# Kernel tuning notes

Measured on AMD Instinct MI355X. Metric: run time of the kernel, lower is better.

## Reference

```python
import jax, jax.numpy as jnp
import numpy as np

N_A, N_G, D, H = 100000, 25000, 128, 4
E_B, E_O, E_R, E_P = 400000, 100000, 200000, 200000
BN_INV = float(1.0 / np.sqrt(1.0 + 1e-5))  # eval-mode BatchNorm1d, running mean 0 / var 1


def setup_inputs():
    key = jax.random.key(0)
    ks = iter(jax.random.split(key, 64))
    nrm = lambda shape, s=0.05: jax.random.normal(next(ks), shape, jnp.float32) * s
    ri = lambda n, hi: jax.random.randint(next(ks), (n,), 0, hi, jnp.int32)
    inp = dict(
        x_atom=nrm((N_A, D), 1.0), x_group=nrm((N_G, D), 1.0),
        ef_bond=nrm((E_B, D), 1.0), ef_overlap=nrm((E_O, D), 1.0),
        bond_src=ri(E_B, N_A), bond_dst=ri(E_B, N_A),
        ov_src=ri(E_O, N_G), ov_dst=ri(E_O, N_G),
        ref_src=ri(E_R, N_G), ref_dst=ri(E_R, N_A),
        pool_src=ri(E_P, N_A), pool_dst=ri(E_P, N_G),
    )
    # two GINE convs (bond 'b', overlap 'o'): eps + MLP Linear(D,2D)->BN->ReLU->Linear(2D,D)
    for pre in ('b', 'o'):
        inp[pre + '_eps'] = jnp.zeros((1,), jnp.float32)
        inp[pre + '_W1'] = nrm((D, 2 * D)); inp[pre + '_b1'] = jnp.zeros((2 * D,), jnp.float32)
        inp[pre + '_g1'] = jnp.ones((2 * D,), jnp.float32); inp[pre + '_be1'] = jnp.zeros((2 * D,), jnp.float32)
        inp[pre + '_W2'] = nrm((2 * D, D)); inp[pre + '_b2'] = jnp.zeros((D,), jnp.float32)
    # two ModifiedGATConvs (refine 'r', pool 'p'): GATConv + Flatten->BN->ReLU->Linear
    for pre in ('r', 'p'):
        inp[pre + '_Wfc'] = nrm((D, H * D)); inp[pre + '_al'] = nrm((H, D)); inp[pre + '_ar'] = nrm((H, D))
        inp[pre + '_Wres'] = nrm((D, H * D)); inp[pre + '_bias'] = jnp.zeros((H * D,), jnp.float32)
        inp[pre + '_g'] = jnp.ones((H * D,), jnp.float32); inp[pre + '_b'] = jnp.zeros((H * D,), jnp.float32)
        inp[pre + '_Wout'] = nrm((H * D, D)); inp[pre + '_bout'] = jnp.zeros((D,), jnp.float32)
    return inp


def _gine(x_src, x_dst, efeat, src, dst, n_dst, eps, W1, b1, g1, be1, W2, b2):
    m = jax.nn.relu(x_src[src] + efeat)                       # [E, D] message: relu(h_src + e)
    neigh = jax.ops.segment_sum(m, dst, num_segments=n_dst)   # [Nd, D] sum-reduce
    h = (1.0 + eps) * x_dst + neigh
    h = h @ W1 + b1
    h = jax.nn.relu(g1 * (h * BN_INV) + be1)                  # eval BN
    return h @ W2 + b2


def _gat(x_src, x_dst, src, dst, n_dst, Wfc, al, ar, Wres, bias, g, b, Wout, bout):
    hs = (x_src @ Wfc).reshape(-1, H, D)                      # [Ns, H, D]
    hd = (x_dst @ Wfc).reshape(-1, H, D)
    el = jnp.sum(hs * al, axis=-1)                            # [Ns, H]
    er = jnp.sum(hd * ar, axis=-1)                            # [Nd, H]
    e = jax.nn.leaky_relu(el[src] + er[dst], 0.2)             # [E, H]
    emax = jax.ops.segment_max(e, dst, num_segments=n_dst)    # per-dst softmax (stable)
    ex = jnp.exp(e - emax[dst])
    den = jax.ops.segment_sum(ex, dst, num_segments=n_dst)
    a = ex / jnp.maximum(den[dst], 1e-9)                      # [E, H]
    rst = jax.ops.segment_sum(a[:, :, None] * hs[src], dst, num_segments=n_dst)  # [Nd, H, D]
    rst = rst + (x_dst @ Wres).reshape(-1, H, D) + bias.reshape(H, D)            # residual + bias
    flat = rst.reshape(-1, H * D)                             # Flatten
    h = jax.nn.relu(g * (flat * BN_INV) + b)                  # eval BN -> ReLU
    return h @ Wout + bout


def reference(x_atom, x_group, ef_bond, ef_overlap, bond_src, bond_dst, ov_src, ov_dst, ref_src, ref_dst, pool_src, pool_dst, b_eps, b_W1, b_b1, b_g1, b_be1, b_W2, b_b2, o_eps, o_W1, o_b1, o_g1, o_be1, o_W2, o_b2, r_Wfc, r_al, r_ar, r_Wres, r_bias, r_g, r_b, r_Wout, r_bout, p_Wfc, p_al, p_ar, p_Wres, p_bias, p_g, p_b, p_Wout, p_bout):
    # HeteroGraphConv with default 'sum' cross-relation aggregation per dst node type
    out_atom = _gine(x_atom, x_atom, ef_bond, bond_src, bond_dst, N_A, b_eps, b_W1, b_b1, b_g1, b_be1, b_W2, b_b2)
    out_atom = out_atom + _gat(x_group, x_atom, ref_src, ref_dst, N_A, r_Wfc, r_al, r_ar, r_Wres, r_bias, r_g, r_b, r_Wout, r_bout)
    out_group = _gine(x_group, x_group, ef_overlap, ov_src, ov_dst, N_G, o_eps, o_W1, o_b1, o_g1, o_be1, o_W2, o_b2)
    out_group = out_group + _gat(x_atom, x_group, pool_src, pool_dst, N_G, p_Wfc, p_al, p_ar, p_Wres, p_bias, p_g, p_b, p_Wout, p_bout)
    return jnp.concatenate([out_atom, out_group], axis=0)     # [N_A + N_G, D]
```

## Files before the change

kernel.cpp:

```cpp
#include <hip/hip_runtime.h>
#include <hip/hip_bf16.h>

#define N_A 100000
#define N_G 25000
#define DD 128
#define E_B 400000
#define E_O 100000
#define E_R 200000
#define E_P 200000
#define EALL 900000
#define NSLOT 250000
#define STRIDE 64

static constexpr float BN_INV_C = 0.99999500003749969f;

typedef __attribute__((ext_vector_type(8))) short bf16x8;
typedef __attribute__((ext_vector_type(4))) float f32x4;

__device__ __forceinline__ unsigned short f2bf(float f) {
    unsigned u = __float_as_uint(f);
    unsigned r = (u + 0x7FFFu + ((u >> 16) & 1u)) >> 16;
    return (unsigned short)r;
}
__device__ __forceinline__ float bf2f(unsigned short s) {
    return __uint_as_float(((unsigned)s) << 16);
}
__device__ __forceinline__ float lrelu(float v) { return v > 0.f ? v : 0.2f * v; }

__global__ void k_xcast_all(const float* __restrict__ xa, const float* __restrict__ xg,
                            unsigned short* __restrict__ xab, unsigned short* __restrict__ xgb) {
    int t = blockIdx.x * blockDim.x + threadIdx.x;
    if (t < N_A * 32) {
        float4 v = *(const float4*)(xa + (size_t)t * 4);
        ushort4 o; o.x = f2bf(v.x); o.y = f2bf(v.y); o.z = f2bf(v.z); o.w = f2bf(v.w);
        *(ushort4*)(xab + (size_t)t * 4) = o;
    } else {
        int t2 = t - N_A * 32;
        if (t2 >= N_G * 32) return;
        float4 v = *(const float4*)(xg + (size_t)t2 * 4);
        ushort4 o; o.x = f2bf(v.x); o.y = f2bf(v.y); o.z = f2bf(v.z); o.w = f2bf(v.w);
        *(ushort4*)(xgb + (size_t)t2 * 4) = o;
    }
}

struct WcSeg { const float* src; unsigned short* dst; int K; int N; int ldk; int off; };
struct WcArgs { WcSeg s[10]; };

__global__ void k_wcast_all(WcArgs a) {
    WcSeg sg = a.s[blockIdx.y];
    int t = blockIdx.x * blockDim.x + threadIdx.x;
    if (t >= sg.K * sg.N) return;
    int n = t % sg.N, k = t / sg.N;
    sg.dst[(size_t)n * sg.ldk + sg.off + k] = f2bf(sg.src[t]);
}

__global__ void k_war_all(const float* __restrict__ rWfc, const float* __restrict__ ral,
                          const float* __restrict__ rar, const float* __restrict__ pWfc,
                          const float* __restrict__ pal, const float* __restrict__ par,
                          float* __restrict__ wv) {
    int bsel = blockIdx.x;
    const float* W = bsel < 2 ? rWfc : pWfc;
    const float* vec = bsel == 0 ? ral : bsel == 1 ? rar : bsel == 2 ? pal : par;
    float* o = wv + bsel * 512;
    int t = threadIdx.x;
    int k = t >> 2, h = t & 3;
    const float* wr = W + (size_t)k * 512 + h * 128;
    const float* av = vec + h * 128;
    float s = 0.f;
    for (int d = 0; d < 128; ++d) s += wr[d] * av[d];
    o[t] = s;
}

__global__ void k_adj_fill(const int* __restrict__ bs, const int* __restrict__ bd,
                           const int* __restrict__ os, const int* __restrict__ od,
                           const int* __restrict__ rs, const int* __restrict__ rd,
                           const int* __restrict__ ps, const int* __restrict__ pd,
                           int* __restrict__ deg, uint2* __restrict__ adj,
                           int* __restrict__ heads, int* __restrict__ nxt) {
    int t = blockIdx.x * blockDim.x + threadIdx.x;
    int e, base, go; const int* S; const int* D;
    if (t < E_B) { e = t; S = bs; D = bd; base = 0; go = 0; }
    else if (t < E_B + E_O) { e = t - E_B; S = os; D = od; base = 100000; go = E_B; }
    else if (t < E_B + E_O + E_R) { e = t - (E_B + E_O); S = rs; D = rd; base = 125000; go = E_B + E_O; }
    else if (t < EALL) { e = t - (E_B + E_O + E_R); S = ps; D = pd; base = 225000; go = E_B + E_O + E_R; }
    else return;
    int d = D[e], s = S[e];
    int ns = base + d;
    int pos = atomicAdd(&deg[ns], 1);
    if (pos < STRIDE) adj[(size_t)ns * STRIDE + pos] = make_uint2((unsigned)e, (unsigned)s);
    else nxt[go + e] = atomicExch(&heads[ns], e);
}

__global__ __launch_bounds__(256) void k_gine_gather_all(
    const unsigned short* __restrict__ xAb, const unsigned short* __restrict__ xGb,
    const float* __restrict__ efB, const float* __restrict__ efO,
    const int* __restrict__ bsrc, const int* __restrict__ osrc,
    const int* __restrict__ deg, const uint2* __restrict__ adj,
    const int* __restrict__ heads, const int* __restrict__ nxt,
    const float* __restrict__ beps, const float* __restrict__ oeps,
    unsigned short* __restrict__ h0A, unsigned short* __restrict__ h0G) {
    int wid = threadIdx.x >> 6, lane = threadIdx.x & 63;
    int n = blockIdx.x * 4 + wid;
    __shared__ uint2 gl[4][STRIDE];
    const unsigned short* xs; const unsigned short* xdrow; const float* ef;
    const int* esrc; const int* nx; float ep; unsigned short* outp; int nn, base, go;
    if (n < N_A) {
        nn = n; xs = xAb; xdrow = xAb + (size_t)n * DD; ef = efB; esrc = bsrc;
        base = 0; go = 0; ep = 1.0f + beps[0]; outp = h0A + (size_t)n * DD;
    } else {
        nn = n - N_A; xs = xGb; xdrow = xGb + (size_t)nn * DD; ef = efO; esrc = osrc;
        base = 100000; go = E_B; ep = 1.0f + oeps[0]; outp = h0G + (size_t)nn * DD;
    }
    nx = nxt + go;
    int d = deg[base + nn];
    int cb = min(d, STRIDE);
    if (lane < cb) gl[wid][lane] = adj[(size_t)(base + nn) * STRIDE + lane];
    __syncthreads();
    float2 acc = make_float2(0.f, 0.f);
    for (int i = 0; i < cb; ++i) {
        uint2 es = gl[wid][i];
        unsigned xa = *(const unsigned*)(xs + (size_t)es.y * DD + lane * 2);
        float2 ev = *(const float2*)(ef + (size_t)es.x * DD + lane * 2);
        acc.x += fmaxf(bf2f((unsigned short)(xa & 0xffff)) + ev.x, 0.f);
        acc.y += fmaxf(bf2f((unsigned short)(xa >> 16)) + ev.y, 0.f);
    }
    if (d > STRIDE) {
        for (int e = heads[base + nn]; e >= 0; e = nx[e]) {
            int s = esrc[e];
            unsigned xa = *(const unsigned*)(xs + (size_t)s * DD + lane * 2);
            float2 ev = *(const float2*)(ef + (size_t)e * DD + lane * 2);
            acc.x += fmaxf(bf2f((unsigned short)(xa & 0xffff)) + ev.x, 0.f);
            acc.y += fmaxf(bf2f((unsigned short)(xa >> 16)) + ev.y, 0.f);
        }
    }
    unsigned xd = *(const unsigned*)(xdrow + lane * 2);
    float rx = ep * bf2f((unsigned short)(xd & 0xffff)) + acc.x;
    float ry = ep * bf2f((unsigned short)(xd >> 16)) + acc.y;
    *(unsigned*)(outp + lane * 2) = (unsigned)f2bf(rx) | ((unsigned)f2bf(ry) << 16);
}

__global__ void k_logit_all(const unsigned short* __restrict__ xAb,
                            const unsigned short* __restrict__ xGb,
                            const float* __restrict__ wv,
                            float* __restrict__ elR, float* __restrict__ elP,
                            float* __restrict__ erR, float* __restrict__ erP) {
    int t = blockIdx.x * blockDim.x + threadIdx.x;
    const unsigned short* xr; const float* wl; const float* wr_; float* ol; float* orr; int idx;
    if (t < N_A * 4) {
        idx = t; xr = xAb + (size_t)(t >> 2) * DD; wl = wv + 1024; wr_ = wv + 512;
        ol = elP; orr = erR;
    } else {
        int t2 = t - N_A * 4;
        if (t2 >= N_G * 4) return;
        idx = t2; xr = xGb + (size_t)(t2 >> 2) * DD; wl = wv; wr_ = wv + 1536;
        ol = elR; orr = erP;
    }
    int h = idx & 3;
    float sl = 0.f, sr = 0.f;
#pragma unroll
    for (int k = 0; k < DD; k += 8) {
        uint4 w = *(const uint4*)(xr + k);
        unsigned wa[4] = {w.x, w.y, w.z, w.w};
#pragma unroll
        for (int q = 0; q < 4; ++q) {
            float x0 = bf2f((unsigned short)(wa[q] & 0xffff));
            float x1 = bf2f((unsigned short)(wa[q] >> 16));
            int k0 = (k + q * 2) * 4 + h, k1 = (k + q * 2 + 1) * 4 + h;
            sl += x0 * wl[k0] + x1 * wl[k1];
            sr += x0 * wr_[k0] + x1 * wr_[k1];
        }
    }
    ol[idx] = sl;
    orr[idx] = sr;
}

__global__ void k_exp_all(const float* __restrict__ elR, const float* __restrict__ erR,
                          const float* __restrict__ elP, const float* __restrict__ erP,
                          const int* __restrict__ rs, const int* __restrict__ rd,
                          const int* __restrict__ ps, const int* __restrict__ pd,
                          float* __restrict__ exR, float* __restrict__ exP,
                          float* __restrict__ denR, float* __restrict__ denP) {
    int t = blockIdx.x * blockDim.x + threadIdx.x;
    if (t < E_R * 4) {
        int e = t >> 2, h = t & 3;
        float v = lrelu(elR[rs[e] * 4 + h] + erR[rd[e] * 4 + h]);
        float x = __expf(v);
        exR[t] = x;
        atomicAdd(&denR[rd[e] * 4 + h], x);
    } else {
        int t2 = t - E_R * 4;
        if (t2 >= E_P * 4) return;
        int e = t2 >> 2, h = t2 & 3;
        float v = lrelu(elP[ps[e] * 4 + h] + erP[pd[e] * 4 + h]);
        float x = __expf(v);
        exP[t2] = x;
        atomicAdd(&denP[pd[e] * 4 + h], x);
    }
}

__global__ __launch_bounds__(256) void k_att_gather_all(
    const unsigned short* __restrict__ xAb, const unsigned short* __restrict__ xGb,
    const float* __restrict__ exR, const float* __restrict__ exP,
    const float* __restrict__ denR, const float* __restrict__ denP,
    const int* __restrict__ rsrc, const int* __restrict__ psrc,
    const int* __restrict__ deg, const uint2* __restrict__ adj,
    const int* __restrict__ heads, const int* __restrict__ nxt,
    unsigned short* __restrict__ A2r, unsigned short* __restrict__ A2p) {
    int wid = threadIdx.x >> 6, lane = threadIdx.x & 63;
    int n = blockIdx.x * 4 + wid;
    __shared__ uint2 gl[4][STRIDE];
    const unsigned short* xs; const float* ex; const float* den;
    const int* esrc; const int* nx; unsigned short* A2; int nn, base, go;
    if (n < N_A) {
        nn = n; xs = xGb; ex = exR; den = denR; esrc = rsrc;
        base = 125000; go = E_B + E_O; A2 = A2r + (size_t)n * 512;
    } else {
        nn = n - N_A; xs = xAb; ex = exP; den = denP; esrc = psrc;
        base = 225000; go = E_B + E_O + E_R; A2 = A2p + (size_t)nn * 512;
    }
    nx = nxt + go;
    int d = deg[base + nn];
    int cb = min(d, STRIDE);
    if (lane < cb) gl[wid][lane] = adj[(size_t)(base + nn) * STRIDE + lane];
    __syncthreads();
    float4 dv = *(const float4*)(den + (size_t)nn * 4);
    float inv0 = 1.f / fmaxf(dv.x, 1e-9f);
    float inv1 = 1.f / fmaxf(dv.y, 1e-9f);
    float inv2 = 1.f / fmaxf(dv.z, 1e-9f);
    float inv3 = 1.f / fmaxf(dv.w, 1e-9f);
    float acc[4][2] = {};
    for (int i = 0; i < cb; ++i) {
        uint2 es = gl[wid][i];
        float4 e4 = *(const float4*)(ex + (size_t)es.x * 4);
        unsigned xw = *(const unsigned*)(xs + (size_t)es.y * DD + lane * 2);
        float x0 = bf2f((unsigned short)(xw & 0xffff));
        float x1 = bf2f((unsigned short)(xw >> 16));
        float a0 = e4.x * inv0, a1 = e4.y * inv1, a2 = e4.z * inv2, a3 = e4.w * inv3;
        acc[0][0] += a0 * x0; acc[0][1] += a0 * x1;
        acc[1][0] += a1 * x0; acc[1][1] += a1 * x1;
        acc[2][0] += a2 * x0; acc[2][1] += a2 * x1;
        acc[3][0] += a3 * x0; acc[3][1] += a3 * x1;
    }
    if (d > STRIDE) {
        for (int e = heads[base + nn]; e >= 0; e = nx[e]) {
            int s = esrc[e];
            float4 e4 = *(const float4*)(ex + (size_t)e * 4);
            unsigned xw = *(const unsigned*)(xs + (size_t)s * DD + lane * 2);
            float x0 = bf2f((unsigned short)(xw & 0xffff));
            float x1 = bf2f((unsigned short)(xw >> 16));
            float a0 = e4.x * inv0, a1 = e4.y * inv1, a2 = e4.z * inv2, a3 = e4.w * inv3;
            acc[0][0] += a0 * x0; acc[0][1] += a0 * x1;
            acc[1][0] += a1 * x0; acc[1][1] += a1 * x1;
            acc[2][0] += a2 * x0; acc[2][1] += a2 * x1;
            acc[3][0] += a3 * x0; acc[3][1] += a3 * x1;
        }
    }
#pragma unroll
    for (int h = 0; h < 4; ++h) {
        unsigned o = (unsigned)f2bf(acc[h][0]) | ((unsigned)f2bf(acc[h][1]) << 16);
        *(unsigned*)(A2 + h * 128 + lane * 2) = o;
    }
}

#define LDKP 40
template <int EPI, int OUTBF, int GATK>
__global__ __launch_bounds__(256) void k_gemm_bf(
    const unsigned short* __restrict__ A, const unsigned short* __restrict__ Bt,
    void* __restrict__ C, int M, int N, int K,
    const float* __restrict__ bias, const float* __restrict__ g,
    const float* __restrict__ be, const unsigned short* __restrict__ addbf,
    const unsigned short* __restrict__ Axd) {
    __shared__ unsigned short As[128 * LDKP];
    __shared__ unsigned short Bs[128 * LDKP];
    int tid = threadIdx.x;
    int wave = tid >> 6, lane = tid & 63;
    int wr = wave >> 1, wc = wave & 1;
    int row0 = blockIdx.y * 128, col0 = blockIdx.x * 128;
    int l16 = lane & 15, khalf = (lane >> 4) * 8;
    f32x4 acc[4][4] = {};
    int r_0 = tid >> 2, ko_0 = (tid & 3) * 8;
    int r_1 = (tid + 256) >> 2, ko_1 = ((tid + 256) & 3) * 8;
    for (int k0 = 0; k0 < K; k0 += 32) {
        __syncthreads();
        {
            int kk = k0 + ko_0;
            int ra = min(row0 + r_0, M - 1);
            uint4 va;
            if (GATK) va = (kk < 128) ? *(const uint4*)(A + (size_t)ra * 512 + col0 + kk)
                                      : *(const uint4*)(Axd + (size_t)ra * 128 + (kk - 128));
            else va = *(const uint4*)(A + (size_t)ra * K + kk);
            *(uint4*)(&As[r_0 * LDKP + ko_0]) = va;
            uint4 vb = *(const uint4*)(Bt + (size_t)(col0 + r_0) * K + kk);
            *(uint4*)(&Bs[r_0 * LDKP + ko_0]) = vb;
            kk = k0 + ko_1;
            ra = min(row0 + r_1, M - 1);
            if (GATK) va = (kk < 128) ? *(const uint4*)(A + (size_t)ra * 512 + col0 + kk)
                                      : *(const uint4*)(Axd + (size_t)ra * 128 + (kk - 128));
            else va = *(const uint4*)(A + (size_t)ra * K + kk);
            *(uint4*)(&As[r_1 * LDKP + ko_1]) = va;
            vb = *(const uint4*)(Bt + (size_t)(col0 + r_1) * K + kk);
            *(uint4*)(&Bs[r_1 * LDKP + ko_1]) = vb;
        }
        __syncthreads();
        bf16x8 af[4], bfr[4];
#pragma unroll
        for (int i = 0; i < 4; ++i)
            af[i] = *(const bf16x8*)(&As[(wr * 64 + i * 16 + l16) * LDKP + khalf]);
#pragma unroll
        for (int j = 0; j < 4; ++j)
            bfr[j] = *(const bf16x8*)(&Bs[(wc * 64 + j * 16 + l16) * LDKP + khalf]);
#pragma unroll
        for (int i = 0; i < 4; ++i)
#pragma unroll
            for (int j = 0; j < 4; ++j)
                acc[i][j] = __builtin_amdgcn_mfma_f32_16x16x32_bf16(af[i], bfr[j], acc[i][j], 0, 0, 0);
    }
    int rq = (lane >> 4) * 4;
#pragma unroll
    for (int i = 0; i < 4; ++i) {
#pragma unroll
        for (int reg = 0; reg < 4; ++reg) {
            int r = row0 + wr * 64 + i * 16 + rq + reg;
            if (r >= M) continue;
#pragma unroll
            for (int j = 0; j < 4; ++j) {
                int c = col0 + wc * 64 + j * 16 + l16;
                float v = acc[i][j][reg];
                size_t idx = (size_t)r * N + c;
                v += bias[c];
                if (EPI == 2) {
                    v = g[c] * (v * BN_INV_C) + be[c];
                    v = fmaxf(v, 0.f);
                }
                if (EPI == 3) {
                    ((float*)C)[idx] = v + bf2f(addbf[idx]);
                } else if (OUTBF) {
                    ((unsigned short*)C)[idx] = f2bf(v);
                } else {
                    ((float*)C)[idx] = v;
                }
            }
        }
    }
}

extern "C" void kernel_launch(void* const* d_in, const int* in_sizes, int n_in,
                              void* d_out, int out_size, void* d_ws, size_t ws_size,
                              hipStream_t stream) {
    const float* x_atom = (const float*)d_in[0];
    const float* x_group = (const float*)d_in[1];
    const float* ef_bond = (const float*)d_in[2];
    const float* ef_ov = (const float*)d_in[3];
    const int* bond_src = (const int*)d_in[4];
    const int* bond_dst = (const int*)d_in[5];
    const int* ov_src = (const int*)d_in[6];
    const int* ov_dst = (const int*)d_in[7];
    const int* ref_src = (const int*)d_in[8];
    const int* ref_dst = (const int*)d_in[9];
    const int* pool_src = (const int*)d_in[10];
    const int* pool_dst = (const int*)d_in[11];
    const float* b_eps = (const float*)d_in[12];
    const float* b_W1 = (const float*)d_in[13];
    const float* b_b1 = (const float*)d_in[14];
    const float* b_g1 = (const float*)d_in[15];
    const float* b_be1 = (const float*)d_in[16];
    const float* b_W2 = (const float*)d_in[17];
    const float* b_b2 = (const float*)d_in[18];
    const float* o_eps = (const float*)d_in[19];
    const float* o_W1 = (const float*)d_in[20];
    const float* o_b1 = (const float*)d_in[21];
    const float* o_g1 = (const float*)d_in[22];
    const float* o_be1 = (const float*)d_in[23];
    const float* o_W2 = (const float*)d_in[24];
    const float* o_b2 = (const float*)d_in[25];
    const float* r_Wfc = (const float*)d_in[26];
    const float* r_al = (const float*)d_in[27];
    const float* r_ar = (const float*)d_in[28];
    const float* r_Wres = (const float*)d_in[29];
    const float* r_bias = (const float*)d_in[30];
    const float* r_g = (const float*)d_in[31];
    const float* r_b = (const float*)d_in[32];
    const float* r_Wout = (const float*)d_in[33];
    const float* r_bout = (const float*)d_in[34];
    const float* p_Wfc = (const float*)d_in[35];
    const float* p_al = (const float*)d_in[36];
    const float* p_ar = (const float*)d_in[37];
    const float* p_Wres = (const float*)d_in[38];
    const float* p_bias = (const float*)d_in[39];
    const float* p_g = (const float*)d_in[40];
    const float* p_b = (const float*)d_in[41];
    const float* p_Wout = (const float*)d_in[42];
    const float* p_bout = (const float*)d_in[43];

    float* out = (float*)d_out;
    char* wsb = (char*)d_ws;
    unsigned short* xAb = (unsigned short*)(wsb + 0);
    unsigned short* xGb = (unsigned short*)(wsb + 26000000);
    unsigned short* WtB1 = (unsigned short*)(wsb + 33000000);
    unsigned short* WtB2 = WtB1 + 32768;
    unsigned short* WtO1 = WtB2 + 32768;
    unsigned short* WtO2 = WtO1 + 32768;
    unsigned short* WtR  = WtO2 + 32768;
    unsigned short* WtRo = WtR + 131072;
    unsigned short* WtP  = WtRo + 65536;
    unsigned short* WtPo = WtP + 131072;
    float* wv   = (float*)(wsb + 34100000);
    int* heads  = (int*)(wsb + 36300000);
    int* nxt    = (int*)(wsb + 37400000);
    unsigned short* h0A = (unsigned short*)(wsb + 41100000);
    unsigned short* h0G = (unsigned short*)(wsb + 66800000);
    unsigned short* R4  = (unsigned short*)(wsb + 73300000);
    unsigned short* G1a = (unsigned short*)(wsb + 124600000);
    unsigned short* G1g = (unsigned short*)(wsb + 150300000);
    unsigned short* A2r = (unsigned short*)(wsb + 156800000);
    unsigned short* A2p = (unsigned short*)(wsb + 259300000);
    unsigned short* R3r = (unsigned short*)(wsb + 285000000);
    unsigned short* R3p = (unsigned short*)(wsb + 387500000);
    uint2* adj  = (uint2*)(wsb + 414000000);
    int* deg    = (int*)(wsb + 543000000);
    float* F    = (float*)(wsb + 544000000);
    float* elR  = F;
    float* elP  = F + 100000;
    float* erR  = F + 500000;
    float* erP  = F + 900000;
    float* denR = F + 1000000;
    float* denP = F + 1400000;
    float* exR  = F + 1500000;
    float* exP  = F + 2300000;

    k_xcast_all<<<((N_A + N_G) * 32 + 255) / 256, 256, 0, stream>>>(x_atom, x_group, xAb, xGb);
    WcArgs wa;
    wa.s[0] = {b_W1, WtB1, 128, 256, 128, 0};
    wa.s[1] = {b_W2, WtB2, 256, 128, 256, 0};
    wa.s[2] = {o_W1, WtO1, 128, 256, 128, 0};
    wa.s[3] = {o_W2, WtO2, 256, 128, 256, 0};
    wa.s[4] = {r_Wfc, WtR, 128, 512, 256, 0};
    wa.s[5] = {r_Wres, WtR, 128, 512, 256, 128};
    wa.s[6] = {r_Wout, WtRo, 512, 128, 512, 0};
    wa.s[7] = {p_Wfc, WtP, 128, 512, 256, 0};
    wa.s[8] = {p_Wres, WtP, 128, 512, 256, 128};
    wa.s[9] = {p_Wout, WtPo, 512, 128, 512, 0};
    k_wcast_all<<<dim3(256, 10), 256, 0, stream>>>(wa);
    k_war_all<<<4, 512, 0, stream>>>(r_Wfc, r_al, r_ar, p_Wfc, p_al, p_ar, wv);
    hipMemsetAsync(deg, 0, NSLOT * 4, stream);
    hipMemsetAsync(heads, 0xFF, NSLOT * 4, stream);
    hipMemsetAsync(denR, 0, 500000 * 4, stream);
    k_adj_fill<<<(EALL + 255) / 256, 256, 0, stream>>>(
        bond_src, bond_dst, ov_src, ov_dst, ref_src, ref_dst, pool_src, pool_dst,
        deg, adj, heads, nxt);
    k_gine_gather_all<<<31250, 256, 0, stream>>>(xAb, xGb, ef_bond, ef_ov, bond_src, ov_src,
                                                 deg, adj, heads, nxt, b_eps, o_eps, h0A, h0G);
    k_gemm_bf<2, 1, 0><<<dim3(2, 782), 256, 0, stream>>>(h0A, WtB1, R4, N_A, 256, 128, b_b1, b_g1, b_be1, nullptr, nullptr);
    k_gemm_bf<1, 1, 0><<<dim3(1, 782), 256, 0, stream>>>(R4, WtB2, G1a, N_A, 128, 256, b_b2, nullptr, nullptr, nullptr, nullptr);
    k_gemm_bf<2, 1, 0><<<dim3(2, 196), 256, 0, stream>>>(h0G, WtO1, R4, N_G, 256, 128, o_b1, o_g1, o_be1, nullptr, nullptr);
    k_gemm_bf<1, 1, 0><<<dim3(1, 196), 256, 0, stream>>>(R4, WtO2, G1g, N_G, 128, 256, o_b2, nullptr, nullptr, nullptr, nullptr);
    k_logit_all<<<((N_A + N_G) * 4 + 255) / 256, 256, 0, stream>>>(xAb, xGb, wv, elR, elP, erR, erP);
    k_exp_all<<<((E_R + E_P) * 4 + 255) / 256, 256, 0, stream>>>(elR, erR, elP, erP,
        ref_src, ref_dst, pool_src, pool_dst, exR, exP, denR, denP);
    k_att_gather_all<<<31250, 256, 0, stream>>>(xAb, xGb, exR, exP, denR, denP, ref_src, pool_src,
                                                deg, adj, heads, nxt, A2r, A2p);
    k_gemm_bf<2, 1, 1><<<dim3(4, 782), 256, 0, stream>>>(A2r, WtR, R3r, N_A, 512, 256, r_bias, r_g, r_b, nullptr, xAb);
    k_gemm_bf<2, 1, 1><<<dim3(4, 196), 256, 0, stream>>>(A2p, WtP, R3p, N_G, 512, 256, p_bias, p_g, p_b, nullptr, xGb);
    k_gemm_bf<3, 0, 0><<<dim3(1, 782), 256, 0, stream>>>(R3r, WtRo, out, N_A, 128, 512, r_bout, nullptr, nullptr, G1a, nullptr);
    k_gemm_bf<3, 0, 0><<<dim3(1, 196), 256, 0, stream>>>(R3p, WtPo, out + (size_t)N_A * DD, N_G, 128, 512, p_bout, nullptr, nullptr, G1g, nullptr);
}
```

Before: 596.8 us.

## Fuse two-layer MLP GEMMs per row block and merge atom/group launches

Replaces the separate first-layer and second-layer GEMM launches with a single kernel per MLP. Each 128-row block computes the hidden activations chunk by chunk into shared memory, applies bias/BN/ReLU, and immediately accumulates the second GEMM. Atom and group problems run in one launch. This removes the round trip of the R4/R3 intermediates through global memory and cuts launch count, at the cost of fewer blocks per launch (each block does all column chunks serially) and more shared memory per block.

```diff
diff --git a/kernel.cpp b/kernel.cpp
--- a/kernel.cpp
+++ b/kernel.cpp
@@ -262,60 +262,99 @@
     }
 }
 
-#define LDKP 40
-template <int EPI, int OUTBF, int GATK>
-__global__ __launch_bounds__(256) void k_gemm_bf(
-    const unsigned short* __restrict__ A, const unsigned short* __restrict__ Bt,
-    void* __restrict__ C, int M, int N, int K,
-    const float* __restrict__ bias, const float* __restrict__ g,
-    const float* __restrict__ be, const unsigned short* __restrict__ addbf,
-    const unsigned short* __restrict__ Axd) {
-    __shared__ unsigned short As[128 * LDKP];
-    __shared__ unsigned short Bs[128 * LDKP];
-    int tid = threadIdx.x;
-    int wave = tid >> 6, lane = tid & 63;
-    int wr = wave >> 1, wc = wave & 1;
-    int row0 = blockIdx.y * 128, col0 = blockIdx.x * 128;
-    int l16 = lane & 15, khalf = (lane >> 4) * 8;
-    f32x4 acc[4][4] = {};
-    int r_0 = tid >> 2, ko_0 = (tid & 3) * 8;
-    int r_1 = (tid + 256) >> 2, ko_1 = ((tid + 256) & 3) * 8;
-    for (int k0 = 0; k0 < K; k0 += 32) {
-        __syncthreads();
-        {
-            int kk = k0 + ko_0;
+#define LDK 40
+#define LDH 136
+template <int GATK>
+__device__ __forceinline__ void mlp_block(
+    const unsigned short* __restrict__ A, const unsigned short* __restrict__ Axd,
+    const unsigned short* __restrict__ W1t, int ldk1,
+    const unsigned short* __restrict__ W2t, int ldk2,
+    const float* __restrict__ b1, const float* __restrict__ g1, const float* __restrict__ be1,
+    const float* __restrict__ b2, const unsigned short* __restrict__ addbf,
+    void* __restrict__ Cptr, int row0, int M, int nch,
+    unsigned short* As, unsigned short* Bs, unsigned short* Hs) {
+    const int tid = threadIdx.x;
+    const int wave = tid >> 6, lane = tid & 63;
+    const int wr = wave >> 1, wc = wave & 1;
+    const int l16 = lane & 15, khalf = (lane >> 4) * 8;
+    const int rq = (lane >> 4) * 4;
+    const int r_0 = tid >> 2, ko = (tid & 3) * 8;
+    const int r_1 = r_0 + 64;
+    const int K1 = GATK ? 256 : 128;
+    f32x4 oacc[4][4] = {};
+    for (int c = 0; c < nch; ++c) {
+        f32x4 hacc[4][4] = {};
+        for (int k0 = 0; k0 < K1; k0 += 32) {
+            __syncthreads();
+            int kk = k0 + ko;
             int ra = min(row0 + r_0, M - 1);
             uint4 va;
-            if (GATK) va = (kk < 128) ? *(const uint4*)(A + (size_t)ra * 512 + col0 + kk)
+            if (GATK) va = (kk < 128) ? *(const uint4*)(A + (size_t)ra * 512 + c * 128 + kk)
                                       : *(const uint4*)(Axd + (size_t)ra * 128 + (kk - 128));
-            else va = *(const uint4*)(A + (size_t)ra * K + kk);
-            *(uint4*)(&As[r_0 * LDKP + ko_0]) = va;
-            uint4 vb = *(const uint4*)(Bt + (size_t)(col0 + r_0) * K + kk);
-            *(uint4*)(&Bs[r_0 * LDKP + ko_0]) = vb;
-            kk = k0 + ko_1;
+            else      va = *(const uint4*)(A + (size_t)ra * 128 + kk);
+            *(uint4*)(&As[r_0 * LDK + ko]) = va;
             ra = min(row0 + r_1, M - 1);
-            if (GATK) va = (kk < 128) ? *(const uint4*)(A + (size_t)ra * 512 + col0 + kk)
+            if (GATK) va = (kk < 128) ? *(const uint4*)(A + (size_t)ra * 512 + c * 128 + kk)
                                       : *(const uint4*)(Axd + (size_t)ra * 128 + (kk - 128));
-            else va = *(const uint4*)(A + (size_t)ra * K + kk);
-            *(uint4*)(&As[r_1 * LDKP + ko_1]) = va;
-            vb = *(const uint4*)(Bt + (size_t)(col0 + r_1) * K + kk);
-            *(uint4*)(&Bs[r_1 * LDKP + ko_1]) = vb;
+            else      va = *(const uint4*)(A + (size_t)ra * 128 + kk);
+            *(uint4*)(&As[r_1 * LDK + ko]) = va;
+            uint4 vb = *(const uint4*)(W1t + (size_t)(c * 128 + r_0) * ldk1 + kk);
+            *(uint4*)(&Bs[r_0 * LDK + ko]) = vb;
+            vb = *(const uint4*)(W1t + (size_t)(c * 128 + r_1) * ldk1 + kk);
+            *(uint4*)(&Bs[r_1 * LDK + ko]) = vb;
+            __syncthreads();
+            bf16x8 af[4], bfr[4];
+#pragma unroll
+            for (int i = 0; i < 4; ++i)
+                af[i] = *(const bf16x8*)(&As[(wr * 64 + i * 16 + l16) * LDK + khalf]);
+#pragma unroll
+            for (int j = 0; j < 4; ++j)
+                bfr[j] = *(const bf16x8*)(&Bs[(wc * 64 + j * 16 + l16) * LDK + khalf]);
+#pragma unroll
+            for (int i = 0; i < 4; ++i)
+#pragma unroll
+                for (int j = 0; j < 4; ++j)
+                    hacc[i][j] = __builtin_amdgcn_mfma_f32_16x16x32_bf16(af[i], bfr[j], hacc[i][j], 0, 0, 0);
         }
         __syncthreads();
-        bf16x8 af[4], bfr[4];
-#pragma unroll
-        for (int i = 0; i < 4; ++i)
-            af[i] = *(const bf16x8*)(&As[(wr * 64 + i * 16 + l16) * LDKP + khalf]);
-#pragma unroll
-        for (int j = 0; j < 4; ++j)
-            bfr[j] = *(const bf16x8*)(&Bs[(wc * 64 + j * 16 + l16) * LDKP + khalf]);
-#pragma unroll
-        for (int i = 0; i < 4; ++i)
+#pragma unroll
+        for (int i = 0; i < 4; ++i) {
+#pragma unroll
+            for (int reg = 0; reg < 4; ++reg) {
+                int rrow = wr * 64 + i * 16 + rq + reg;
+#pragma unroll
+                for (int j = 0; j < 4; ++j) {
+                    int ccol = wc * 64 + j * 16 + l16;
+                    int ch = c * 128 + ccol;
+                    float v = hacc[i][j][reg] + b1[ch];
+                    v = g1[ch] * (v * BN_INV_C) + be1[ch];
+                    Hs[rrow * LDH + ccol] = f2bf(fmaxf(v, 0.f));
+                }
+            }
+        }
+        __syncthreads();
+        for (int k0 = 0; k0 < 128; k0 += 32) {
+            __syncthreads();
+            int kk = c * 128 + k0 + ko;
+            uint4 vb = *(const uint4*)(W2t + (size_t)r_0 * ldk2 + kk);
+            *(uint4*)(&Bs[r_0 * LDK + ko]) = vb;
+            vb = *(const uint4*)(W2t + (size_t)r_1 * ldk2 + kk);
+            *(uint4*)(&Bs[r_1 * LDK + ko]) = vb;
+            __syncthreads();
+            bf16x8 af[4], bfr[4];
+#pragma unroll
+            for (int i = 0; i < 4; ++i)
+                af[i] = *(const bf16x8*)(&Hs[(wr * 64 + i * 16 + l16) * LDH + k0 + khalf]);
 #pragma unroll
             for (int j = 0; j < 4; ++j)
-                acc[i][j] = __builtin_amdgcn_mfma_f32_16x16x32_bf16(af[i], bfr[j], acc[i][j], 0, 0, 0);
-    }
-    int rq = (lane >> 4) * 4;
+                bfr[j] = *(const bf16x8*)(&Bs[(wc * 64 + j * 16 + l16) * LDK + khalf]);
+#pragma unroll
+            for (int i = 0; i < 4; ++i)
+#pragma unroll
+                for (int j = 0; j < 4; ++j)
+                    oacc[i][j] = __builtin_amdgcn_mfma_f32_16x16x32_bf16(af[i], bfr[j], oacc[i][j], 0, 0, 0);
+        }
+    }
 #pragma unroll
     for (int i = 0; i < 4; ++i) {
 #pragma unroll
@@ -324,24 +363,61 @@
             if (r >= M) continue;
 #pragma unroll
             for (int j = 0; j < 4; ++j) {
-                int c = col0 + wc * 64 + j * 16 + l16;
-                float v = acc[i][j][reg];
-                size_t idx = (size_t)r * N + c;
-                v += bias[c];
-                if (EPI == 2) {
-                    v = g[c] * (v * BN_INV_C) + be[c];
-                    v = fmaxf(v, 0.f);
-                }
-                if (EPI == 3) {
-                    ((float*)C)[idx] = v + bf2f(addbf[idx]);
-                } else if (OUTBF) {
-                    ((unsigned short*)C)[idx] = f2bf(v);
-                } else {
-                    ((float*)C)[idx] = v;
-                }
+                int cc = wc * 64 + j * 16 + l16;
+                size_t idx = (size_t)r * 128 + cc;
+                float v = oacc[i][j][reg] + b2[cc];
+                if (GATK) ((float*)Cptr)[idx] = v + bf2f(addbf[idx]);
+                else ((unsigned short*)Cptr)[idx] = f2bf(v);
             }
         }
     }
+}
+
+#define NBA 782
+#define NBG 196
+
+__global__ __launch_bounds__(256) void k_gine_mlp(
+    const unsigned short* __restrict__ h0A, const unsigned short* __restrict__ h0G,
+    const unsigned short* __restrict__ WtB1, const unsigned short* __restrict__ WtB2,
+    const unsigned short* __restrict__ WtO1, const unsigned short* __restrict__ WtO2,
+    const float* __restrict__ bb1, const float* __restrict__ bg1, const float* __restrict__ bbe1,
+    const float* __restrict__ bb2,
+    const float* __restrict__ ob1, const float* __restrict__ og1, const float* __restrict__ obe1,
+    const float* __restrict__ ob2,
+    unsigned short* __restrict__ G1a, unsigned short* __restrict__ G1g) {
+    __shared__ unsigned short As[128 * LDK];
+    __shared__ unsigned short Bs[128 * LDK];
+    __shared__ unsigned short Hs[128 * LDH];
+    int bx = blockIdx.x;
+    if (bx < NBA)
+        mlp_block<0>(h0A, nullptr, WtB1, 128, WtB2, 256, bb1, bg1, bbe1, bb2, nullptr,
+                     G1a, bx * 128, N_A, 2, As, Bs, Hs);
+    else
+        mlp_block<0>(h0G, nullptr, WtO1, 128, WtO2, 256, ob1, og1, obe1, ob2, nullptr,
+                     G1g, (bx - NBA) * 128, N_G, 2, As, Bs, Hs);
+}
+
+__global__ __launch_bounds__(256) void k_gat_mlp(
+    const unsigned short* __restrict__ A2r, const unsigned short* __restrict__ A2p,
+    const unsigned short* __restrict__ xAb, const unsigned short* __restrict__ xGb,
+    const unsigned short* __restrict__ WtR, const unsigned short* __restrict__ WtRo,
+    const unsigned short* __restrict__ WtP, const unsigned short* __restrict__ WtPo,
+    const float* __restrict__ rbias, const float* __restrict__ rg, const float* __restrict__ rb,
+    const float* __restrict__ rbout,
+    const float* __restrict__ pbias, const float* __restrict__ pg, const float* __restrict__ pb,
+    const float* __restrict__ pbout,
+    const unsigned short* __restrict__ G1a, const unsigned short* __restrict__ G1g,
+    float* __restrict__ out) {
+    __shared__ unsigned short As[128 * LDK];
+    __shared__ unsigned short Bs[128 * LDK];
+    __shared__ unsigned short Hs[128 * LDH];
+    int bx = blockIdx.x;
+    if (bx < NBA)
+        mlp_block<1>(A2r, xAb, WtR, 256, WtRo, 512, rbias, rg, rb, rbout, G1a,
+                     out, bx * 128, N_A, 4, As, Bs, Hs);
+    else
+        mlp_block<1>(A2p, xGb, WtP, 256, WtPo, 512, pbias, pg, pb, pbout, G1g,
+                     out + (size_t)N_A * DD, (bx - NBA) * 128, N_G, 4, As, Bs, Hs);
 }
 
 extern "C" void kernel_launch(void* const* d_in, const int* in_sizes, int n_in,
@@ -409,13 +485,10 @@
     int* nxt    = (int*)(wsb + 37400000);
     unsigned short* h0A = (unsigned short*)(wsb + 41100000);
     unsigned short* h0G = (unsigned short*)(wsb + 66800000);
-    unsigned short* R4  = (unsigned short*)(wsb + 73300000);
     unsigned short* G1a = (unsigned short*)(wsb + 124600000);
     unsigned short* G1g = (unsigned short*)(wsb + 150300000);
     unsigned short* A2r = (unsigned short*)(wsb + 156800000);
     unsigned short* A2p = (unsigned short*)(wsb + 259300000);
-    unsigned short* R3r = (unsigned short*)(wsb + 285000000);
-    unsigned short* R3p = (unsigned short*)(wsb + 387500000);
     uint2* adj  = (uint2*)(wsb + 414000000);
     int* deg    = (int*)(wsb + 543000000);
     float* F    = (float*)(wsb + 544000000);
@@ -450,17 +523,15 @@
         deg, adj, heads, nxt);
     k_gine_gather_all<<<31250, 256, 0, stream>>>(xAb, xGb, ef_bond, ef_ov, bond_src, ov_src,
                                                  deg, adj, heads, nxt, b_eps, o_eps, h0A, h0G);
-    k_gemm_bf<2, 1, 0><<<dim3(2, 782), 256, 0, stream>>>(h0A, WtB1, R4, N_A, 256, 128, b_b1, b_g1, b_be1, nullptr, nullptr);
-    k_gemm_bf<1, 1, 0><<<dim3(1, 782), 256, 0, stream>>>(R4, WtB2, G1a, N_A, 128, 256, b_b2, nullptr, nullptr, nullptr, nullptr);
-    k_gemm_bf<2, 1, 0><<<dim3(2, 196), 256, 0, stream>>>(h0G, WtO1, R4, N_G, 256, 128, o_b1, o_g1, o_be1, nullptr, nullptr);
-    k_gemm_bf<1, 1, 0><<<dim3(1, 196), 256, 0, stream>>>(R4, WtO2, G1g, N_G, 128, 256, o_b2, nullptr, nullptr, nullptr, nullptr);
+    k_gine_mlp<<<NBA + NBG, 256, 0, stream>>>(h0A, h0G, WtB1, WtB2, WtO1, WtO2,
+                                              b_b1, b_g1, b_be1, b_b2, o_b1, o_g1, o_be1, o_b2,
+                                              G1a, G1g);
     k_logit_all<<<((N_A + N_G) * 4 + 255) / 256, 256, 0, stream>>>(xAb, xGb, wv, elR, elP, erR, erP);
     k_exp_all<<<((E_R + E_P) * 4 + 255) / 256, 256, 0, stream>>>(elR, erR, elP, erP,
         ref_src, ref_dst, pool_src, pool_dst, exR, exP, denR, denP);
     k_att_gather_all<<<31250, 256, 0, stream>>>(xAb, xGb, exR, exP, denR, denP, ref_src, pool_src,
                                                 deg, adj, heads, nxt, A2r, A2p);
-    k_gemm_bf<2, 1, 1><<<dim3(4, 782), 256, 0, stream>>>(A2r, WtR, R3r, N_A, 512, 256, r_bias, r_g, r_b, nullptr, xAb);
-    k_gemm_bf<2, 1, 1><<<dim3(4, 196), 256, 0, stream>>>(A2p, WtP, R3p, N_G, 512, 256, p_bias, p_g, p_b, nullptr, xGb);
-    k_gemm_bf<3, 0, 0><<<dim3(1, 782), 256, 0, stream>>>(R3r, WtRo, out, N_A, 128, 512, r_bout, nullptr, nullptr, G1a, nullptr);
-    k_gemm_bf<3, 0, 0><<<dim3(1, 196), 256, 0, stream>>>(R3p, WtPo, out + (size_t)N_A * DD, N_G, 128, 512, p_bout, nullptr, nullptr, G1g, nullptr);
-}
+    k_gat_mlp<<<NBA + NBG, 256, 0, stream>>>(A2r, A2p, xAb, xGb, WtR, WtRo, WtP, WtPo,
+                                             r_bias, r_g, r_b, r_bout, p_bias, p_g, p_b, p_bout,
+                                             G1a, G1g, out);
+}
```

After: 619.2 us. +3.7%, slower.
